# Performance work log

Measured on AMD Instinct MI355X. Metric: run time of the kernel, lower is better.

## Reference

```python
import jax, jax.numpy as jnp
import numpy as np

N_NODES = 100000
N_EDGES = 1600000


def _sage_conv(x, src, dst, Wl, bl, Wr):
    # mean aggregation of source features into destination nodes
    msg_sum = jax.ops.segment_sum(x[src], dst, num_segments=N_NODES)  # [N, d]
    deg = jax.ops.segment_sum(jnp.ones((src.shape[0],), x.dtype), dst,
                              num_segments=N_NODES)
    agg = msg_sum / jnp.maximum(deg, 1.0)[:, None]
    # PyG SAGEConv: lin_l on aggregated neighbors (with bias), lin_r on root
    return agg @ Wl.T + bl + x @ Wr.T


def setup_inputs() -> dict:
    key = jax.random.key(0)
    ks = jax.random.split(key, 8)
    d_in, d_h, n_cls = 128, 128, 40
    s = lambda fan_in: 1.0 / np.sqrt(fan_in)
    return {
        "x": jax.random.normal(ks[0], (N_NODES, d_in), jnp.float32),
        "edge_index": jax.random.randint(ks[1], (2, N_EDGES), 0, N_NODES,
                                         dtype=jnp.int64),
        "Wl1": jax.random.normal(ks[2], (d_h, d_in), jnp.float32) * s(d_in),
        "bl1": jax.random.normal(ks[3], (d_h,), jnp.float32) * s(d_in),
        "Wr1": jax.random.normal(ks[4], (d_h, d_in), jnp.float32) * s(d_in),
        "Wl2": jax.random.normal(ks[5], (n_cls, d_h), jnp.float32) * s(d_h),
        "bl2": jax.random.normal(ks[6], (n_cls,), jnp.float32) * s(d_h),
        "Wr2": jax.random.normal(ks[7], (n_cls, d_h), jnp.float32) * s(d_h),
    }


def reference(x, edge_index, Wl1, bl1, Wr1, Wl2, bl2, Wr2):
    src, dst = edge_index[0], edge_index[1]
    h = _sage_conv(x, src, dst, Wl1, bl1, Wr1)
    h = jax.nn.relu(h)
    return _sage_conv(h, src, dst, Wl2, bl2, Wr2)
```

## Files before the change

### kernel.cpp

```cpp
#include <hip/hip_runtime.h>
#include <stdint.h>

#define NN 100000
#define NE 1600000
#define NBLK 256
#define BSH 7
#define NBUK ((NN + 127) >> 7)
#define NH (NBUK * NBLK)

typedef _Float16 half8 __attribute__((ext_vector_type(8)));
typedef _Float16 half4 __attribute__((ext_vector_type(4)));
typedef float f32x4 __attribute__((ext_vector_type(4)));

__device__ inline float2 unpack_h2(unsigned v) {
    union { unsigned u; _Float16 h[2]; } c; c.u = v;
    return make_float2((float)c.h[0], (float)c.h[1]);
}
__device__ inline unsigned pack_h2(float a, float b) {
    union { unsigned u; _Float16 h[2]; } c;
    c.h[0] = (_Float16)a; c.h[1] = (_Float16)b; return c.u;
}


__global__ __launch_bounds__(256) void k_hist(const int* __restrict__ ei,
                                              int* __restrict__ histM) {
    __shared__ int h[NBUK];
    for (int i = threadIdx.x; i < NBUK; i += 256) h[i] = 0;
    __syncthreads();
    int blk = blockIdx.x;
    int chunk = (NE + NBLK - 1) / NBLK;
    int beg = blk * chunk;
    int end = beg + chunk < NE ? beg + chunk : NE;
    for (int e = beg + threadIdx.x; e < end; e += 256)
        atomicAdd(&h[ei[NE + e] >> BSH], 1);
    __syncthreads();
    for (int b = threadIdx.x; b < NBUK; b += 256)
        histM[b * NBLK + blk] = h[b];
}

__global__ __launch_bounds__(512) void k_scan1(int* __restrict__ data,
                                               int* __restrict__ partial, int n) {
    __shared__ int s[512];
    int t = threadIdx.x;
    int i = blockIdx.x * 512 + t;
    int v = (i < n) ? data[i] : 0;
    s[t] = v;
    __syncthreads();
    #pragma unroll
    for (int off = 1; off < 512; off <<= 1) {
        int tmp = (t >= off) ? s[t - off] : 0;
        __syncthreads();
        s[t] += tmp;
        __syncthreads();
    }
    if (i < n) data[i] = s[t];
    if (t == 511) partial[blockIdx.x] = s[511];
}

__global__ void k_scanout(const int* __restrict__ incl, const int* __restrict__ partial,
                          int* __restrict__ offM, int n) {
    int i = blockIdx.x * blockDim.x + threadIdx.x;
    if (i < n) {
        int b = i >> 9;
        int off = b ? partial[b - 1] : 0;
        offM[i + 1] = incl[i] + off;
        if (i == 0) offM[0] = 0;
    }
}

__global__ __launch_bounds__(256) void k_scatter(const int* __restrict__ ei,
                                                 const int* __restrict__ offM,
                                                 unsigned* __restrict__ pairs) {
    __shared__ int cur[NBUK];
    int blk = blockIdx.x;
    for (int b = threadIdx.x; b < NBUK; b += 256)
        cur[b] = offM[b * NBLK + blk];
    __syncthreads();
    int chunk = (NE + NBLK - 1) / NBLK;
    int beg = blk * chunk;
    int end = beg + chunk < NE ? beg + chunk : NE;
    for (int e = beg + threadIdx.x; e < end; e += 256) {
        int d = ei[NE + e];
        int s = ei[e];
        int pos = atomicAdd(&cur[d >> BSH], 1);
        pairs[pos] = ((unsigned)s << BSH) | (unsigned)(d & 127);
    }
}

__global__ __launch_bounds__(256) void k_csr(const unsigned* __restrict__ pairs,
                                             const int* __restrict__ offM,
                                             int* __restrict__ csr,
                                             int* __restrict__ row_ptr) {
    __shared__ int cnt[128], off[129], cur[128];
    int b = blockIdx.x;
    int t = threadIdx.x;
    int ebeg = offM[b * NBLK];
    int eend = (b + 1 < NBUK) ? offM[(b + 1) * NBLK] : NE;
    if (t < 128) cnt[t] = 0;
    __syncthreads();
    for (int e = ebeg + t; e < eend; e += 256)
        atomicAdd(&cnt[pairs[e] & 127], 1);
    __syncthreads();
    if (t == 0) {
        int acc = 0;
        for (int i = 0; i < 128; ++i) { off[i] = acc; acc += cnt[i]; }
        off[128] = acc;
    }
    __syncthreads();
    if (t < 128) cur[t] = 0;
    __syncthreads();
    for (int e = ebeg + t; e < eend; e += 256) {
        unsigned p = pairs[e];
        int local = p & 127;
        int lpos = atomicAdd(&cur[local], 1);
        csr[ebeg + off[local] + lpos] = (int)(p >> BSH);
    }
    int n0 = b << BSH;
    if (t < 128 && n0 + t < NN) row_ptr[n0 + t] = ebeg + off[t];
    if (b == 0 && t == 0) row_ptr[NN] = NE;
}


__global__ void k_prep_w(const float* __restrict__ Wl1, const float* __restrict__ Wr1,
                         const float* __restrict__ Wl2, const float* __restrict__ Wr2,
                         _Float16* __restrict__ Wc1, _Float16* __restrict__ Wc2) {
    int i = blockIdx.x * 256 + threadIdx.x;
    if (i < 16384) {
        Wc1[i] = (_Float16)Wl1[i];
        Wc1[16384 + i] = (_Float16)Wr1[i];
    }
    if (i < 5120) {
        Wc2[i] = (_Float16)Wl2[i];
        Wc2[5120 + i] = (_Float16)Wr2[i];
    }
}


template <int A_F32>
__global__ __launch_bounds__(256) void k_gemm(const void* __restrict__ Av,
                                              const _Float16* __restrict__ W,
                                              _Float16* __restrict__ C,
                                              int M, int Ntot) {
    __shared__ _Float16 As[64][136];
    __shared__ _Float16 Ws[64][136];
    int tid = threadIdx.x;
    int m0 = blockIdx.x * 64;

    if (A_F32) {
        const float* A = (const float*)Av;
        #pragma unroll
        for (int it = 0; it < 8; ++it) {
            int idx = it * 1024 + tid * 4;
            int r = idx >> 7, c = idx & 127;
            float4 v = make_float4(0.f, 0.f, 0.f, 0.f);
            if (m0 + r < M) v = *(const float4*)&A[(size_t)(m0 + r) * 128 + c];
            half4 hv;
            hv[0] = (_Float16)v.x; hv[1] = (_Float16)v.y;
            hv[2] = (_Float16)v.z; hv[3] = (_Float16)v.w;
            *(half4*)&As[r][c] = hv;
        }
    } else {
        const _Float16* A = (const _Float16*)Av;
        #pragma unroll
        for (int it = 0; it < 4; ++it) {
            int idx = it * 2048 + tid * 8;
            int r = idx >> 7, c = idx & 127;
            half8 v = {};
            if (m0 + r < M) v = *(const half8*)&A[(size_t)(m0 + r) * 128 + c];
            *(half8*)&As[r][c] = v;
        }
    }

    int wave = tid >> 6, lane = tid & 63;
    int wm = (wave >> 1) * 32, wn = (wave & 1) * 32;
    int lrow = lane & 15, kblk = lane >> 4;

    for (int nc0 = 0; nc0 < Ntot; nc0 += 64) {
        __syncthreads();
        #pragma unroll
        for (int it = 0; it < 4; ++it) {
            int idx = it * 2048 + tid * 8;
            int r = idx >> 7, c = idx & 127;
            half8 v = {};
            if (nc0 + r < Ntot) v = *(const half8*)&W[(size_t)(nc0 + r) * 128 + c];
            *(half8*)&Ws[r][c] = v;
        }
        __syncthreads();

        f32x4 acc00 = {0.f,0.f,0.f,0.f}, acc01 = {0.f,0.f,0.f,0.f};
        f32x4 acc10 = {0.f,0.f,0.f,0.f}, acc11 = {0.f,0.f,0.f,0.f};
        #pragma unroll
        for (int ks = 0; ks < 4; ++ks) {
            half8 a0 = *(const half8*)&As[wm + lrow][ks * 32 + kblk * 8];
            half8 a1 = *(const half8*)&As[wm + 16 + lrow][ks * 32 + kblk * 8];
            half8 b0 = *(const half8*)&Ws[wn + lrow][ks * 32 + kblk * 8];
            half8 b1 = *(const half8*)&Ws[wn + 16 + lrow][ks * 32 + kblk * 8];
            acc00 = __builtin_amdgcn_mfma_f32_16x16x32_f16(a0, b0, acc00, 0, 0, 0);
            acc01 = __builtin_amdgcn_mfma_f32_16x16x32_f16(a0, b1, acc01, 0, 0, 0);
            acc10 = __builtin_amdgcn_mfma_f32_16x16x32_f16(a1, b0, acc10, 0, 0, 0);
            acc11 = __builtin_amdgcn_mfma_f32_16x16x32_f16(a1, b1, acc11, 0, 0, 0);
        }

        int rbase = kblk * 4;
        #pragma unroll
        for (int r = 0; r < 4; ++r) {
            int gr0 = m0 + wm + rbase + r;
            int gr1 = m0 + wm + 16 + rbase + r;
            int gc0 = nc0 + wn + lrow;
            int gc1 = nc0 + wn + 16 + lrow;
            if (gr0 < M && gc0 < Ntot) C[(size_t)gr0 * Ntot + gc0] = (_Float16)acc00[r];
            if (gr0 < M && gc1 < Ntot) C[(size_t)gr0 * Ntot + gc1] = (_Float16)acc01[r];
            if (gr1 < M && gc0 < Ntot) C[(size_t)gr1 * Ntot + gc0] = (_Float16)acc10[r];
            if (gr1 < M && gc1 < Ntot) C[(size_t)gr1 * Ntot + gc1] = (_Float16)acc11[r];
        }
    }
}


__global__ __launch_bounds__(256) void k_agg1(const _Float16* __restrict__ tmp1,
                                              const float* __restrict__ bl1,
                                              const int* __restrict__ row_ptr,
                                              const int* __restrict__ csr,
                                              _Float16* __restrict__ h) {
    int node = blockIdx.x * 4 + (threadIdx.x >> 6);
    if (node >= NN) return;
    int lane = threadIdx.x & 63;
    int beg = row_ptr[node], end = row_ptr[node + 1];
    const unsigned* p = (const unsigned*)tmp1;
    float sx = 0.f, sy = 0.f;
    int e = beg;
    for (; e + 8 <= end; e += 8) {
        int s0 = csr[e],     s1 = csr[e + 1], s2 = csr[e + 2], s3 = csr[e + 3];
        int s4 = csr[e + 4], s5 = csr[e + 5], s6 = csr[e + 6], s7 = csr[e + 7];
        unsigned v0 = p[(size_t)s0 * 128 + lane];
        unsigned v1 = p[(size_t)s1 * 128 + lane];
        unsigned v2 = p[(size_t)s2 * 128 + lane];
        unsigned v3 = p[(size_t)s3 * 128 + lane];
        unsigned v4 = p[(size_t)s4 * 128 + lane];
        unsigned v5 = p[(size_t)s5 * 128 + lane];
        unsigned v6 = p[(size_t)s6 * 128 + lane];
        unsigned v7 = p[(size_t)s7 * 128 + lane];
        float2 f0 = unpack_h2(v0), f1 = unpack_h2(v1);
        float2 f2 = unpack_h2(v2), f3 = unpack_h2(v3);
        sx += (f0.x + f1.x) + (f2.x + f3.x);
        sy += (f0.y + f1.y) + (f2.y + f3.y);
        float2 f4 = unpack_h2(v4), f5 = unpack_h2(v5);
        float2 f6 = unpack_h2(v6), f7 = unpack_h2(v7);
        sx += (f4.x + f5.x) + (f6.x + f7.x);
        sy += (f4.y + f5.y) + (f6.y + f7.y);
    }
    for (; e + 4 <= end; e += 4) {
        int s0 = csr[e], s1 = csr[e + 1], s2 = csr[e + 2], s3 = csr[e + 3];
        float2 f0 = unpack_h2(p[(size_t)s0 * 128 + lane]);
        float2 f1 = unpack_h2(p[(size_t)s1 * 128 + lane]);
        float2 f2 = unpack_h2(p[(size_t)s2 * 128 + lane]);
        float2 f3 = unpack_h2(p[(size_t)s3 * 128 + lane]);
        sx += (f0.x + f1.x) + (f2.x + f3.x);
        sy += (f0.y + f1.y) + (f2.y + f3.y);
    }
    for (; e < end; ++e) {
        float2 f = unpack_h2(p[(size_t)csr[e] * 128 + lane]);
        sx += f.x; sy += f.y;
    }
    int deg = end - beg;
    float inv = 1.0f / (float)(deg > 1 ? deg : 1);
    float2 xr = unpack_h2(p[(size_t)node * 128 + 64 + lane]);
    float2 b = *(const float2*)&bl1[lane * 2];
    float o0 = fmaxf(sx * inv + b.x + xr.x, 0.f);
    float o1 = fmaxf(sy * inv + b.y + xr.y, 0.f);
    ((unsigned*)h)[(size_t)node * 64 + lane] = pack_h2(o0, o1);
}


__global__ __launch_bounds__(256) void k_agg2(const _Float16* __restrict__ tmp2,
                                              const float* __restrict__ bl2,
                                              const int* __restrict__ row_ptr,
                                              const int* __restrict__ csr,
                                              float* __restrict__ out) {
    int tid = threadIdx.x;
    int wave = tid >> 6, lane = tid & 63;
    int hw = lane >> 5, ln = lane & 31;
    int node = blockIdx.x * 8 + wave * 2 + hw;
    bool act = (node < NN) && (ln < 20);
    int beg = 0, end = 0;
    if (node < NN) { beg = row_ptr[node]; end = row_ptr[node + 1]; }
    const unsigned* p = (const unsigned*)tmp2;
    float sx = 0.f, sy = 0.f;
    int e = beg;
    for (; e + 8 <= end; e += 8) {
        int s0 = csr[e],     s1 = csr[e + 1], s2 = csr[e + 2], s3 = csr[e + 3];
        int s4 = csr[e + 4], s5 = csr[e + 5], s6 = csr[e + 6], s7 = csr[e + 7];
        if (act) {
            unsigned v0 = p[(size_t)s0 * 40 + ln];
            unsigned v1 = p[(size_t)s1 * 40 + ln];
            unsigned v2 = p[(size_t)s2 * 40 + ln];
            unsigned v3 = p[(size_t)s3 * 40 + ln];
            unsigned v4 = p[(size_t)s4 * 40 + ln];
            unsigned v5 = p[(size_t)s5 * 40 + ln];
            unsigned v6 = p[(size_t)s6 * 40 + ln];
            unsigned v7 = p[(size_t)s7 * 40 + ln];
            float2 f0 = unpack_h2(v0), f1 = unpack_h2(v1);
            float2 f2 = unpack_h2(v2), f3 = unpack_h2(v3);
            sx += (f0.x + f1.x) + (f2.x + f3.x);
            sy += (f0.y + f1.y) + (f2.y + f3.y);
            float2 f4 = unpack_h2(v4), f5 = unpack_h2(v5);
            float2 f6 = unpack_h2(v6), f7 = unpack_h2(v7);
            sx += (f4.x + f5.x) + (f6.x + f7.x);
            sy += (f4.y + f5.y) + (f6.y + f7.y);
        }
    }
    for (; e + 4 <= end; e += 4) {
        int s0 = csr[e], s1 = csr[e + 1], s2 = csr[e + 2], s3 = csr[e + 3];
        if (act) {
            float2 f0 = unpack_h2(p[(size_t)s0 * 40 + ln]);
            float2 f1 = unpack_h2(p[(size_t)s1 * 40 + ln]);
            float2 f2 = unpack_h2(p[(size_t)s2 * 40 + ln]);
            float2 f3 = unpack_h2(p[(size_t)s3 * 40 + ln]);
            sx += (f0.x + f1.x) + (f2.x + f3.x);
            sy += (f0.y + f1.y) + (f2.y + f3.y);
        }
    }
    for (; e < end; ++e) {
        int s = csr[e];
        if (act) {
            float2 f = unpack_h2(p[(size_t)s * 40 + ln]);
            sx += f.x; sy += f.y;
        }
    }
    if (act) {
        int deg = end - beg;
        float inv = 1.0f / (float)(deg > 1 ? deg : 1);
        float2 hr = unpack_h2(p[(size_t)node * 40 + 20 + ln]);
        float2 b = *(const float2*)&bl2[ln * 2];
        float2 o;
        o.x = sx * inv + b.x + hr.x;
        o.y = sy * inv + b.y + hr.y;
        *(float2*)&out[(size_t)node * 40 + ln * 2] = o;
    }
}


extern "C" void kernel_launch(void* const* d_in, const int* in_sizes, int n_in,
                              void* d_out, int out_size, void* d_ws, size_t ws_size,
                              hipStream_t stream) {
    const float* x   = (const float*)d_in[0];
    const int* ei    = (const int*)d_in[1];
    const float* Wl1 = (const float*)d_in[2];
    const float* bl1 = (const float*)d_in[3];
    const float* Wr1 = (const float*)d_in[4];
    const float* Wl2 = (const float*)d_in[5];
    const float* bl2 = (const float*)d_in[6];
    const float* Wr2 = (const float*)d_in[7];
    float* out = (float*)d_out;

    char* ws = (char*)d_ws;
    size_t off = 0;
    auto alloc = [&](size_t bytes) -> char* {
        char* pp = ws + off;
        off = (off + bytes + 511) & ~(size_t)511;
        return pp;
    };
    int* histM      = (int*)alloc((size_t)NH * 4);
    int* offM       = (int*)alloc((size_t)(NH + 1) * 4);
    int* partial    = (int*)alloc(1024 * 4);
    int* partial2   = (int*)alloc(1024 * 4);
    unsigned* pairs = (unsigned*)alloc((size_t)NE * 4);
    int* csr        = (int*)alloc((size_t)NE * 4);
    int* row_ptr    = (int*)alloc((size_t)(NN + 1) * 4);
    _Float16* Wc1   = (_Float16*)alloc((size_t)256 * 128 * 2);
    _Float16* Wc2   = (_Float16*)alloc((size_t)80 * 128 * 2);
    _Float16* tmp1  = (_Float16*)alloc((size_t)NN * 256 * 2);
    _Float16* h     = (_Float16*)alloc((size_t)NN * 128 * 2);
    _Float16* tmp2  = (_Float16*)alloc((size_t)NN * 80 * 2);
    if (off > ws_size) return;

    k_hist<<<NBLK, 256, 0, stream>>>(ei, histM);
    int NSB = (NH + 511) / 512;
    k_scan1<<<NSB, 512, 0, stream>>>(histM, partial, NH);
    k_scan1<<<1, 512, 0, stream>>>(partial, partial2, NSB);
    k_scanout<<<(NH + 255) / 256, 256, 0, stream>>>(histM, partial, offM, NH);
    k_scatter<<<NBLK, 256, 0, stream>>>(ei, offM, pairs);
    k_csr<<<NBUK, 256, 0, stream>>>(pairs, offM, csr, row_ptr);

    k_prep_w<<<64, 256, 0, stream>>>(Wl1, Wr1, Wl2, Wr2, Wc1, Wc2);

    int gm = (NN + 63) / 64;
    k_gemm<1><<<gm, 256, 0, stream>>>(x, Wc1, tmp1, NN, 256);
    k_agg1<<<(NN + 3) / 4, 256, 0, stream>>>(tmp1, bl1, row_ptr, csr, h);
    k_gemm<0><<<gm, 256, 0, stream>>>(h, Wc2, tmp2, NN, 80);
    k_agg2<<<(NN + 7) / 8, 256, 0, stream>>>(tmp2, bl2, row_ptr, csr, out);
}
```

Measured before the change: 312.3 us.

## Split agg1 feature columns across two grid halves with half-wave edge parallelism

The first-layer aggregation kernel now launches twice as many blocks. Each block handles one half of the feature columns, and each wave's two 32-lane halves process alternating edges, combining their sums with a cross-lane shuffle. Each gather now reads 128 bytes per row per half-wave instead of 256 bytes per wave. The aim is more memory-level parallelism and more waves in flight for the irregular gather. In exchange, row_ptr and csr indices are read twice, there is an extra shuffle, and the epilogue is done by only half the lanes.

```diff
diff --git a/kernel.cpp b/kernel.cpp
--- a/kernel.cpp
+++ b/kernel.cpp
@@ -222,24 +222,34 @@
                                               const int* __restrict__ row_ptr,
                                               const int* __restrict__ csr,
                                               _Float16* __restrict__ h) {
-    int node = blockIdx.x * 4 + (threadIdx.x >> 6);
+    int NB = (NN + 3) / 4;
+    int bx = blockIdx.x;
+    int c0h = 0;
+    if (bx >= NB) { bx -= NB; c0h = 32; }
+    int tid = threadIdx.x;
+    int node = bx * 4 + (tid >> 6);
     if (node >= NN) return;
-    int lane = threadIdx.x & 63;
+    int lane = tid & 63;
+    int hw = lane >> 5;
+    int ln = lane & 31;
+    int col = c0h + ln;
     int beg = row_ptr[node], end = row_ptr[node + 1];
     const unsigned* p = (const unsigned*)tmp1;
     float sx = 0.f, sy = 0.f;
     int e = beg;
-    for (; e + 8 <= end; e += 8) {
-        int s0 = csr[e],     s1 = csr[e + 1], s2 = csr[e + 2], s3 = csr[e + 3];
-        int s4 = csr[e + 4], s5 = csr[e + 5], s6 = csr[e + 6], s7 = csr[e + 7];
-        unsigned v0 = p[(size_t)s0 * 128 + lane];
-        unsigned v1 = p[(size_t)s1 * 128 + lane];
-        unsigned v2 = p[(size_t)s2 * 128 + lane];
-        unsigned v3 = p[(size_t)s3 * 128 + lane];
-        unsigned v4 = p[(size_t)s4 * 128 + lane];
-        unsigned v5 = p[(size_t)s5 * 128 + lane];
-        unsigned v6 = p[(size_t)s6 * 128 + lane];
-        unsigned v7 = p[(size_t)s7 * 128 + lane];
+    for (; e + 16 <= end; e += 16) {
+        int s0 = csr[e + 0 + hw],  s1 = csr[e + 2 + hw];
+        int s2 = csr[e + 4 + hw],  s3 = csr[e + 6 + hw];
+        int s4 = csr[e + 8 + hw],  s5 = csr[e + 10 + hw];
+        int s6 = csr[e + 12 + hw], s7 = csr[e + 14 + hw];
+        unsigned v0 = p[(size_t)s0 * 128 + col];
+        unsigned v1 = p[(size_t)s1 * 128 + col];
+        unsigned v2 = p[(size_t)s2 * 128 + col];
+        unsigned v3 = p[(size_t)s3 * 128 + col];
+        unsigned v4 = p[(size_t)s4 * 128 + col];
+        unsigned v5 = p[(size_t)s5 * 128 + col];
+        unsigned v6 = p[(size_t)s6 * 128 + col];
+        unsigned v7 = p[(size_t)s7 * 128 + col];
         float2 f0 = unpack_h2(v0), f1 = unpack_h2(v1);
         float2 f2 = unpack_h2(v2), f3 = unpack_h2(v3);
         sx += (f0.x + f1.x) + (f2.x + f3.x);
@@ -249,26 +259,26 @@
         sx += (f4.x + f5.x) + (f6.x + f7.x);
         sy += (f4.y + f5.y) + (f6.y + f7.y);
     }
-    for (; e + 4 <= end; e += 4) {
-        int s0 = csr[e], s1 = csr[e + 1], s2 = csr[e + 2], s3 = csr[e + 3];
-        float2 f0 = unpack_h2(p[(size_t)s0 * 128 + lane]);
-        float2 f1 = unpack_h2(p[(size_t)s1 * 128 + lane]);
-        float2 f2 = unpack_h2(p[(size_t)s2 * 128 + lane]);
-        float2 f3 = unpack_h2(p[(size_t)s3 * 128 + lane]);
-        sx += (f0.x + f1.x) + (f2.x + f3.x);
-        sy += (f0.y + f1.y) + (f2.y + f3.y);
-    }
-    for (; e < end; ++e) {
-        float2 f = unpack_h2(p[(size_t)csr[e] * 128 + lane]);
+    for (; e + 2 <= end; e += 2) {
+        int s = csr[e + hw];
+        float2 f = unpack_h2(p[(size_t)s * 128 + col]);
         sx += f.x; sy += f.y;
     }
-    int deg = end - beg;
-    float inv = 1.0f / (float)(deg > 1 ? deg : 1);
-    float2 xr = unpack_h2(p[(size_t)node * 128 + 64 + lane]);
-    float2 b = *(const float2*)&bl1[lane * 2];
-    float o0 = fmaxf(sx * inv + b.x + xr.x, 0.f);
-    float o1 = fmaxf(sy * inv + b.y + xr.y, 0.f);
-    ((unsigned*)h)[(size_t)node * 64 + lane] = pack_h2(o0, o1);
+    if (e < end && hw == 0) {
+        float2 f = unpack_h2(p[(size_t)csr[e] * 128 + col]);
+        sx += f.x; sy += f.y;
+    }
+    sx += __shfl_xor(sx, 32, 64);
+    sy += __shfl_xor(sy, 32, 64);
+    if (hw == 0) {
+        int deg = end - beg;
+        float inv = 1.0f / (float)(deg > 1 ? deg : 1);
+        float2 xr = unpack_h2(p[(size_t)node * 128 + 64 + col]);
+        float2 b = *(const float2*)&bl1[col * 2];
+        float o0 = fmaxf(sx * inv + b.x + xr.x, 0.f);
+        float o1 = fmaxf(sy * inv + b.y + xr.y, 0.f);
+        ((unsigned*)h)[(size_t)node * 64 + col] = pack_h2(o0, o1);
+    }
 }
 
 
@@ -386,7 +396,8 @@
 
     int gm = (NN + 63) / 64;
     k_gemm<1><<<gm, 256, 0, stream>>>(x, Wc1, tmp1, NN, 256);
-    k_agg1<<<(NN + 3) / 4, 256, 0, stream>>>(tmp1, bl1, row_ptr, csr, h);
+    int NB1a = (NN + 3) / 4;
+    k_agg1<<<2 * NB1a, 256, 0, stream>>>(tmp1, bl1, row_ptr, csr, h);
     k_gemm<0><<<gm, 256, 0, stream>>>(h, Wc2, tmp2, NN, 80);
     k_agg2<<<(NN + 7) / 8, 256, 0, stream>>>(tmp2, bl2, row_ptr, csr, out);
 }
```

After: 351.7 us. 1.13x slower.
